# Optimization experiments

Hardware: AMD Instinct MI355X
Metric: run time of the kernel (lower is better)

Reference implementation:

```python
import jax, jax.numpy as jnp
import numpy as np

NUM_HEADS = 16
LN_EPS = 1e-05


def setup_inputs() -> dict:
    key = jax.random.key(0)
    ks = jax.random.split(key, 10)
    B, S, H = 2, 2048, 1024
    s = 1.0 / np.sqrt(H)
    return {
        "hidden_states": jax.random.normal(ks[0], (B, S, H), dtype=jnp.float32),
        "Wq": jax.random.normal(ks[1], (H, H), dtype=jnp.float32) * s,
        "bq": jax.random.normal(ks[2], (H,), dtype=jnp.float32) * 0.02,
        "Wk": jax.random.normal(ks[3], (H, H), dtype=jnp.float32) * s,
        "bk": jax.random.normal(ks[4], (H,), dtype=jnp.float32) * 0.02,
        "Wv": jax.random.normal(ks[5], (H, H), dtype=jnp.float32) * s,
        "bv": jax.random.normal(ks[6], (H,), dtype=jnp.float32) * 0.02,
        "Wd": jax.random.normal(ks[7], (H, H), dtype=jnp.float32) * s,
        "bd": jax.random.normal(ks[8], (H,), dtype=jnp.float32) * 0.02,
        "ln_gamma": jnp.ones((H,), dtype=jnp.float32),
        "ln_beta": jnp.zeros((H,), dtype=jnp.float32),
    }


def reference(hidden_states, Wq, bq, Wk, bk, Wv, bv, Wd, bd, ln_gamma, ln_beta):
    B, S, H = hidden_states.shape
    nh = NUM_HEADS
    hd = H // nh

    # QKV projections (torch Linear: x @ W.T + b), split heads -> [B, nh, S, hd]
    def proj(W, b):
        y = jnp.einsum('bsh,oh->bso', hidden_states, W) + b
        return y.reshape(B, S, nh, hd).transpose(0, 2, 1, 3)

    q = proj(Wq, bq)
    k = proj(Wk, bk)
    v = proj(Wv, bv)

    # scaled dot-product attention: [B, nh, S, S]
    scores = jnp.einsum('bhqd,bhkd->bhqk', q, k) / jnp.sqrt(jnp.float32(hd))
    probs = jax.nn.softmax(scores, axis=-1)
    ctx = jnp.einsum('bhqk,bhkd->bhqd', probs, v)  # [B, nh, S, hd]
    ctx = ctx.transpose(0, 2, 1, 3).reshape(B, S, H)

    # output dense + residual + LayerNorm
    attn_out = jnp.einsum('bsh,oh->bso', ctx, Wd) + bd
    x = attn_out + hidden_states
    mu = jnp.mean(x, axis=-1, keepdims=True)
    var = jnp.mean(jnp.square(x - mu), axis=-1, keepdims=True)
    return (x - mu) * jax.lax.rsqrt(var + LN_EPS) * ln_gamma + ln_beta
```

## Files before the change

kernel.cpp:

```cpp
#include <hip/hip_runtime.h>

constexpr int kH    = 1024;
constexpr int kSEQ  = 2048;
constexpr int kBATCH= 2;
constexpr int kNH   = 16;
constexpr int kHD   = 64;
constexpr int kM    = 4096;

typedef _Float16 h8  __attribute__((ext_vector_type(8)));
typedef _Float16 h4  __attribute__((ext_vector_type(4)));
typedef float   f32x4 __attribute__((ext_vector_type(4)));

static __device__ __forceinline__ f32x4 mfma16(h8 a, h8 b, f32x4 c) {
  return __builtin_amdgcn_mfma_f32_16x16x32_f16(a, b, c, 0, 0, 0);
}

static __device__ __forceinline__ void gll16(const _Float16* g, _Float16* l) {
  __builtin_amdgcn_global_load_lds(
      (const __attribute__((address_space(1))) void*)g,
      (__attribute__((address_space(3))) void*)l, 16, 0, 0);
}

#define QSCALE 0.18033688011112042f
#define C0INIT (-5.770780163555854f)

__global__ __launch_bounds__(256) void cvt_all(
    const float* __restrict__ X,  const float* __restrict__ Wq,
    const float* __restrict__ Wk, const float* __restrict__ Wv,
    const float* __restrict__ Wd,
    _Float16* __restrict__ Xh,  _Float16* __restrict__ Wqh,
    _Float16* __restrict__ Wkh, _Float16* __restrict__ Wvh,
    _Float16* __restrict__ Wdh)
{
  int i = blockIdx.x * 256 + threadIdx.x;
  const float* src; _Float16* dst; int off;
  if (i < (kM * kH) / 4) {
    src = X; dst = Xh; off = i;
  } else {
    int j = i - (kM * kH) / 4;
    int w = j >> 18;
    off = j & 262143;
    src = (w == 0) ? Wq : (w == 1) ? Wk : (w == 2) ? Wv : Wd;
    dst = (w == 0) ? Wqh : (w == 1) ? Wkh : (w == 2) ? Wvh : Wdh;
  }
  float4 v = reinterpret_cast<const float4*>(src)[off];
  h4 o;
  o[0] = (_Float16)v.x; o[1] = (_Float16)v.y;
  o[2] = (_Float16)v.z; o[3] = (_Float16)v.w;
  reinterpret_cast<h4*>(dst)[off] = o;
}

__global__ __launch_bounds__(256) void qkv_gemm(
    const _Float16* __restrict__ Xh,
    const _Float16* __restrict__ Wq, const _Float16* __restrict__ Wk,
    const _Float16* __restrict__ Wv,
    const float* __restrict__ bq, const float* __restrict__ bk,
    const float* __restrict__ bv,
    _Float16* __restrict__ Qo, _Float16* __restrict__ Ko, _Float16* __restrict__ Vo)
{
  const int proj = blockIdx.z;
  const _Float16* W   = (proj == 0) ? Wq : ((proj == 1) ? Wk : Wv);
  const float*    bias= (proj == 0) ? bq : ((proj == 1) ? bk : bv);
  _Float16*       Out = (proj == 0) ? Qo : ((proj == 1) ? Ko : Vo);

  const int m0 = blockIdx.y * 128, n0 = blockIdx.x * 128;
  __shared__ __align__(16) _Float16 As[128 * 32];
  __shared__ __align__(16) _Float16 Bs[128 * 32];

  const int tid  = threadIdx.x;
  const int wave = tid >> 6, lane = tid & 63, quad = lane >> 4, l16 = lane & 15;
  const int mw = (wave & 1) * 64, nw = (wave >> 1) * 64;

  f32x4 acc[4][4] = {};
  const int grow = wave * 32 + (lane >> 2);
  const int gcol = (lane & 3) * 8;
  const _Float16* Ag = Xh + (size_t)(m0 + grow) * kH + gcol;
  const _Float16* Bg = W  + (size_t)(n0 + grow) * kH + gcol;
  _Float16* AsW = As + wave * 1024;
  _Float16* BsW = Bs + wave * 1024;

  for (int k0 = 0; k0 < kH; k0 += 32) {
    gll16(Ag + k0,            AsW);
    gll16(Ag + 16 * kH + k0,  AsW + 512);
    gll16(Bg + k0,            BsW);
    gll16(Bg + 16 * kH + k0,  BsW + 512);
    __syncthreads();
    h8 af[4], bf[4];
    #pragma unroll
    for (int mi = 0; mi < 4; ++mi)
      af[mi] = *reinterpret_cast<const h8*>(&As[(mw + mi * 16 + l16) * 32 + quad * 8]);
    #pragma unroll
    for (int ni = 0; ni < 4; ++ni)
      bf[ni] = *reinterpret_cast<const h8*>(&Bs[(nw + ni * 16 + l16) * 32 + quad * 8]);
    #pragma unroll
    for (int mi = 0; mi < 4; ++mi)
      #pragma unroll
      for (int ni = 0; ni < 4; ++ni)
        acc[mi][ni] = mfma16(af[mi], bf[ni], acc[mi][ni]);
    __syncthreads();
  }

  #pragma unroll
  for (int mi = 0; mi < 4; ++mi)
  #pragma unroll
  for (int ni = 0; ni < 4; ++ni) {
    const int ng = n0 + nw + ni * 16 + l16;
    const float bv_ = bias[ng];
    const int hh = ng >> 6, dd = ng & 63;
    #pragma unroll
    for (int r = 0; r < 4; ++r) {
      const int mg = m0 + mw + mi * 16 + quad * 4 + r;
      float val = acc[mi][ni][r] + bv_;
      if (proj == 0) val *= QSCALE;
      const int bb = mg >> 11, srow = mg & 2047;
      Out[(((size_t)(bb * kNH + hh) * kSEQ) + srow) * kHD + dd] = (_Float16)val;
    }
  }
}

__global__ __launch_bounds__(256) void vtrans(const _Float16* __restrict__ V,
                                              _Float16* __restrict__ Vt)
{
  const int st = blockIdx.x;
  const int bh = blockIdx.y;
  __shared__ __align__(16) _Float16 Lt[64][72];
  const int t = threadIdx.x, r = t >> 2, c = (t & 3) * 16;
  const _Float16* src = V + (size_t)bh * kSEQ * kHD + (size_t)(st * 64 + r) * kHD + c;
  h8 p0 = *reinterpret_cast<const h8*>(src);
  h8 p1 = *reinterpret_cast<const h8*>(src + 8);
  #pragma unroll
  for (int e = 0; e < 8; ++e) Lt[c + e][r] = p0[e];
  #pragma unroll
  for (int e = 0; e < 8; ++e) Lt[c + 8 + e][r] = p1[e];
  __syncthreads();
  _Float16* dst = Vt + (size_t)bh * kHD * kSEQ + (size_t)r * kSEQ + st * 64 + c;
  *reinterpret_cast<h8*>(dst)     = *reinterpret_cast<const h8*>(&Lt[r][c]);
  *reinterpret_cast<h8*>(dst + 8) = *reinterpret_cast<const h8*>(&Lt[r][c + 8]);
}

__global__ __launch_bounds__(256, 2) void attn_kernel(
    const _Float16* __restrict__ Q, const _Float16* __restrict__ K,
    const _Float16* __restrict__ Vt, _Float16* __restrict__ Ctx)
{
  const int qt = blockIdx.x, bh = blockIdx.y;
  const int tid = threadIdx.x;
  const int wave = tid >> 6, lane = tid & 63, quad = lane >> 4, l16 = lane & 15;
  const int sw = l16 & 7;

  __shared__ __align__(16) _Float16 Kl[128 * 64];
  __shared__ __align__(16) _Float16 Vl[64 * 128];
  __shared__ __align__(16) _Float16 Pl[4 * 32 * 128];

  const _Float16* Qb = Q  + (size_t)bh * kSEQ * kHD;
  const _Float16* Kb = K  + (size_t)bh * kSEQ * kHD;
  const _Float16* Vb = Vt + (size_t)bh * kHD * kSEQ;

  const int qbase = qt * 128 + wave * 32;
  h8 qf[2][2];
  #pragma unroll
  for (int qh = 0; qh < 2; ++qh)
    #pragma unroll
    for (int dh = 0; dh < 2; ++dh)
      qf[qh][dh] = *reinterpret_cast<const h8*>(
          &Qb[(size_t)(qbase + qh * 16 + l16) * kHD + dh * 32 + quad * 8]);

  const int krow = wave * 32 + (lane >> 3);
  const int kcg  = (lane & 7) ^ ((lane >> 3) & 7);
  const _Float16* Kg0 = Kb + (size_t)krow * kHD + kcg * 8;
  _Float16* KlW = Kl + wave * 2048;
  const int vrow = wave * 16 + (lane >> 4);
  _Float16* VlW = Vl + wave * 2048;
  _Float16* PlW = Pl + wave * (32 * 128);

  float l_acc0 = 0.f, l_acc1 = 0.f;
  f32x4 o[2][4] = {};

  for (int kt = 0; kt < kSEQ / 128; ++kt) {
    __syncthreads();
    #pragma unroll
    for (int i = 0; i < 4; ++i)
      gll16(Kg0 + (size_t)kt * (128 * 64) + i * (8 * 64), KlW + i * 512);
    #pragma unroll
    for (int i = 0; i < 4; ++i) {
      const int d = vrow + i * 4;
      const int c = (lane & 15) ^ (d & 7);
      gll16(Vb + (size_t)d * kSEQ + kt * 128 + c * 8, VlW + i * 512);
    }
    __syncthreads();

    f32x4 s[8][2];
    #pragma unroll
    for (int nt = 0; nt < 8; ++nt) {
      const int keyl = nt * 16 + l16;
      h8 ka0 = *reinterpret_cast<const h8*>(&Kl[keyl * 64 + ((quad    ) ^ sw) * 8]);
      h8 ka1 = *reinterpret_cast<const h8*>(&Kl[keyl * 64 + ((quad + 4) ^ sw) * 8]);
      #pragma unroll
      for (int qh = 0; qh < 2; ++qh) {
        f32x4 a = {C0INIT, C0INIT, C0INIT, C0INIT};
        a = mfma16(ka0, qf[qh][0], a);
        a = mfma16(ka1, qf[qh][1], a);
        s[nt][qh] = a;
      }
    }
    #pragma unroll
    for (int nt = 0; nt < 8; ++nt)
      #pragma unroll
      for (int qh = 0; qh < 2; ++qh) {
        float e0 = exp2f(s[nt][qh][0]);
        float e1 = exp2f(s[nt][qh][1]);
        float e2 = exp2f(s[nt][qh][2]);
        float e3 = exp2f(s[nt][qh][3]);
        float t4 = (e0 + e1) + (e2 + e3);
        if (qh == 0) l_acc0 += t4; else l_acc1 += t4;
        h4 pp;
        pp[0] = (_Float16)e0; pp[1] = (_Float16)e1;
        pp[2] = (_Float16)e2; pp[3] = (_Float16)e3;
        const int c16 = (nt * 2 + (quad >> 1)) ^ sw;
        *reinterpret_cast<h4*>(
            &PlW[(qh * 16 + l16) * 128 + c16 * 8 + (quad & 1) * 4]) = pp;
      }
    #pragma unroll
    for (int kc = 0; kc < 4; ++kc) {
      const int cs = ((kc * 4 + quad) ^ sw) * 8;
      h8 pa0 = *reinterpret_cast<const h8*>(&PlW[l16 * 128 + cs]);
      h8 pa1 = *reinterpret_cast<const h8*>(&PlW[(16 + l16) * 128 + cs]);
      #pragma unroll
      for (int dt = 0; dt < 4; ++dt) {
        h8 vbf = *reinterpret_cast<const h8*>(&Vl[(dt * 16 + l16) * 128 + cs]);
        o[0][dt] = mfma16(pa0, vbf, o[0][dt]);
        o[1][dt] = mfma16(pa1, vbf, o[1][dt]);
      }
    }
  }

  float li[2] = {l_acc0, l_acc1};
  #pragma unroll
  for (int qh = 0; qh < 2; ++qh) {
    li[qh] += __shfl_xor(li[qh], 16);
    li[qh] += __shfl_xor(li[qh], 32);
    li[qh] = 1.f / li[qh];
  }
  const int b = bh >> 4, hh = bh & 15;
  #pragma unroll
  for (int qh = 0; qh < 2; ++qh)
    #pragma unroll
    for (int r = 0; r < 4; ++r) {
      const float linv = __shfl(li[qh], quad * 4 + r);
      const int srow = qbase + qh * 16 + quad * 4 + r;
      #pragma unroll
      for (int dt = 0; dt < 4; ++dt) {
        const int col = hh * kHD + dt * 16 + l16;
        Ctx[((size_t)(b * kSEQ + srow)) * kH + col] =
            (_Float16)(o[qh][dt][r] * linv);
      }
    }
}

__global__ __launch_bounds__(256) void dense_gemm(
    const _Float16* __restrict__ A, const _Float16* __restrict__ W,
    const float* __restrict__ bias, const float* __restrict__ resid,
    float* __restrict__ Out)
{
  const int m0 = blockIdx.y * 128, n0 = blockIdx.x * 128;
  __shared__ __align__(16) _Float16 As[128 * 32];
  __shared__ __align__(16) _Float16 Bs[128 * 32];
  const int tid  = threadIdx.x;
  const int wave = tid >> 6, lane = tid & 63, quad = lane >> 4, l16 = lane & 15;
  const int mw = (wave & 1) * 64, nw = (wave >> 1) * 64;
  f32x4 acc[4][4] = {};
  const int grow = wave * 32 + (lane >> 2);
  const int gcol = (lane & 3) * 8;
  const _Float16* Ag = A + (size_t)(m0 + grow) * kH + gcol;
  const _Float16* Bg = W + (size_t)(n0 + grow) * kH + gcol;
  _Float16* AsW = As + wave * 1024;
  _Float16* BsW = Bs + wave * 1024;

  for (int k0 = 0; k0 < kH; k0 += 32) {
    gll16(Ag + k0,           AsW);
    gll16(Ag + 16 * kH + k0, AsW + 512);
    gll16(Bg + k0,           BsW);
    gll16(Bg + 16 * kH + k0, BsW + 512);
    __syncthreads();
    h8 af[4], bf[4];
    #pragma unroll
    for (int mi = 0; mi < 4; ++mi)
      af[mi] = *reinterpret_cast<const h8*>(&As[(mw + mi * 16 + l16) * 32 + quad * 8]);
    #pragma unroll
    for (int ni = 0; ni < 4; ++ni)
      bf[ni] = *reinterpret_cast<const h8*>(&Bs[(nw + ni * 16 + l16) * 32 + quad * 8]);
    #pragma unroll
    for (int mi = 0; mi < 4; ++mi)
      #pragma unroll
      for (int ni = 0; ni < 4; ++ni)
        acc[mi][ni] = mfma16(af[mi], bf[ni], acc[mi][ni]);
    __syncthreads();
  }
  #pragma unroll
  for (int mi = 0; mi < 4; ++mi)
  #pragma unroll
  for (int ni = 0; ni < 4; ++ni) {
    const int ng = n0 + nw + ni * 16 + l16;
    const float bv_ = bias[ng];
    #pragma unroll
    for (int r = 0; r < 4; ++r) {
      const int mg = m0 + mw + mi * 16 + quad * 4 + r;
      Out[(size_t)mg * kH + ng] = acc[mi][ni][r] + bv_ + resid[(size_t)mg * kH + ng];
    }
  }
}

__global__ __launch_bounds__(256) void ln_kernel(const float* __restrict__ Tmp,
    const float* __restrict__ gamma, const float* __restrict__ beta,
    float* __restrict__ out)
{
  const int row = blockIdx.x;
  const float4 v = reinterpret_cast<const float4*>(Tmp + (size_t)row * kH)[threadIdx.x];
  float s  = v.x + v.y + v.z + v.w;
  float ss = v.x * v.x + v.y * v.y + v.z * v.z + v.w * v.w;
  #pragma unroll
  for (int off = 32; off > 0; off >>= 1) {
    s  += __shfl_down(s, off);
    ss += __shfl_down(ss, off);
  }
  __shared__ float red[8];
  const int wave = threadIdx.x >> 6, lane = threadIdx.x & 63;
  if (lane == 0) { red[wave] = s; red[4 + wave] = ss; }
  __syncthreads();
  s  = red[0] + red[1] + red[2] + red[3];
  ss = red[4] + red[5] + red[6] + red[7];
  const float mu   = s * (1.f / kH);
  const float var  = ss * (1.f / kH) - mu * mu;
  const float rstd = rsqrtf(var + 1e-5f);
  const float4 g  = reinterpret_cast<const float4*>(gamma)[threadIdx.x];
  const float4 bb = reinterpret_cast<const float4*>(beta)[threadIdx.x];
  float4 o;
  o.x = (v.x - mu) * rstd * g.x + bb.x;
  o.y = (v.y - mu) * rstd * g.y + bb.y;
  o.z = (v.z - mu) * rstd * g.z + bb.z;
  o.w = (v.w - mu) * rstd * g.w + bb.w;
  reinterpret_cast<float4*>(out + (size_t)row * kH)[threadIdx.x] = o;
}

extern "C" void kernel_launch(void* const* d_in, const int* in_sizes, int n_in,
                              void* d_out, int out_size, void* d_ws, size_t ws_size,
                              hipStream_t stream) {
  const float* hs    = (const float*)d_in[0];
  const float* Wq    = (const float*)d_in[1];
  const float* bq    = (const float*)d_in[2];
  const float* Wk    = (const float*)d_in[3];
  const float* bk    = (const float*)d_in[4];
  const float* Wv    = (const float*)d_in[5];
  const float* bv    = (const float*)d_in[6];
  const float* Wd    = (const float*)d_in[7];
  const float* bd    = (const float*)d_in[8];
  const float* gamma = (const float*)d_in[9];
  const float* beta  = (const float*)d_in[10];
  float* out = (float*)d_out;

  char* ws = (char*)d_ws;
  _Float16* Xh  = (_Float16*)(ws + 0);
  _Float16* Wqh = (_Float16*)(ws + 8388608);
  _Float16* Wkh = (_Float16*)(ws + 10485760);
  _Float16* Wvh = (_Float16*)(ws + 12582912);
  _Float16* Wdh = (_Float16*)(ws + 14680064);
  _Float16* Qh  = (_Float16*)(ws + 16777216);
  _Float16* Kh  = (_Float16*)(ws + 25165824);
  _Float16* Vh  = (_Float16*)(ws + 33554432);
  _Float16* Ch  = (_Float16*)(ws + 41943040);
  _Float16* Vtb = Xh;
  float*    Tmp = (float*)Qh;

  cvt_all<<<8192, 256, 0, stream>>>(hs, Wq, Wk, Wv, Wd, Xh, Wqh, Wkh, Wvh, Wdh);
  qkv_gemm<<<dim3(kH / 128, kM / 128, 3), 256, 0, stream>>>(
      Xh, Wqh, Wkh, Wvh, bq, bk, bv, Qh, Kh, Vh);
  vtrans<<<dim3(kSEQ / 64, kBATCH * kNH), 256, 0, stream>>>(Vh, Vtb);
  attn_kernel<<<dim3(kSEQ / 128, kBATCH * kNH), 256, 0, stream>>>(Qh, Kh, Vtb, Ch);
  dense_gemm<<<dim3(kH / 128, kM / 128), 256, 0, stream>>>(Ch, Wdh, bd, hs, Tmp);
  ln_kernel<<<kM, 256, 0, stream>>>(Tmp, gamma, beta, out);
}
```

Baseline: 237.4 us.

## Double-buffer LDS tiles in GEMMs and attention, shrink attention key tile

Both the QKV and dense GEMM kernels now double-buffer their A/B shared-memory tiles. The next k-slice is prefetched with global_load_lds right after a single barrier, replacing the previous load-sync-compute-sync loop. The attention kernel halves its key tile from 128 to 64, double-buffers the K and V tiles with the same prefetch pattern, and raises its occupancy hint from 2 to 3 blocks. The aim is to overlap global loads with MFMA work and cut barriers. In exchange the GEMMs use twice the LDS, the attention kernel runs twice as many loop iterations, and tighter launch bounds may pressure registers.

```diff
diff --git a/kernel.cpp b/kernel.cpp
--- a/kernel.cpp
+++ b/kernel.cpp
@@ -50,7 +50,7 @@
   reinterpret_cast<h4*>(dst)[off] = o;
 }
 
-__global__ __launch_bounds__(256) void qkv_gemm(
+__global__ __launch_bounds__(256, 2) void qkv_gemm(
     const _Float16* __restrict__ Xh,
     const _Float16* __restrict__ Wq, const _Float16* __restrict__ Wk,
     const _Float16* __restrict__ Wv,
@@ -64,8 +64,8 @@
   _Float16*       Out = (proj == 0) ? Qo : ((proj == 1) ? Ko : Vo);
 
   const int m0 = blockIdx.y * 128, n0 = blockIdx.x * 128;
-  __shared__ __align__(16) _Float16 As[128 * 32];
-  __shared__ __align__(16) _Float16 Bs[128 * 32];
+  __shared__ __align__(16) _Float16 As[2][128 * 32];
+  __shared__ __align__(16) _Float16 Bs[2][128 * 32];
 
   const int tid  = threadIdx.x;
   const int wave = tid >> 6, lane = tid & 63, quad = lane >> 4, l16 = lane & 15;
@@ -76,28 +76,36 @@
   const int gcol = (lane & 3) * 8;
   const _Float16* Ag = Xh + (size_t)(m0 + grow) * kH + gcol;
   const _Float16* Bg = W  + (size_t)(n0 + grow) * kH + gcol;
-  _Float16* AsW = As + wave * 1024;
-  _Float16* BsW = Bs + wave * 1024;
-
-  for (int k0 = 0; k0 < kH; k0 += 32) {
-    gll16(Ag + k0,            AsW);
-    gll16(Ag + 16 * kH + k0,  AsW + 512);
-    gll16(Bg + k0,            BsW);
-    gll16(Bg + 16 * kH + k0,  BsW + 512);
+
+  {
+    gll16(Ag,            &As[0][wave * 1024]);
+    gll16(Ag + 16 * kH,  &As[0][wave * 1024 + 512]);
+    gll16(Bg,            &Bs[0][wave * 1024]);
+    gll16(Bg + 16 * kH,  &Bs[0][wave * 1024 + 512]);
+  }
+
+  for (int k = 0; k < 32; ++k) {
+    const int cur = k & 1;
     __syncthreads();
+    if (k < 31) {
+      const int k0 = (k + 1) * 32, nb = cur ^ 1;
+      gll16(Ag + k0,           &As[nb][wave * 1024]);
+      gll16(Ag + 16 * kH + k0, &As[nb][wave * 1024 + 512]);
+      gll16(Bg + k0,           &Bs[nb][wave * 1024]);
+      gll16(Bg + 16 * kH + k0, &Bs[nb][wave * 1024 + 512]);
+    }
     h8 af[4], bf[4];
     #pragma unroll
     for (int mi = 0; mi < 4; ++mi)
-      af[mi] = *reinterpret_cast<const h8*>(&As[(mw + mi * 16 + l16) * 32 + quad * 8]);
+      af[mi] = *reinterpret_cast<const h8*>(&As[cur][(mw + mi * 16 + l16) * 32 + quad * 8]);
     #pragma unroll
     for (int ni = 0; ni < 4; ++ni)
-      bf[ni] = *reinterpret_cast<const h8*>(&Bs[(nw + ni * 16 + l16) * 32 + quad * 8]);
+      bf[ni] = *reinterpret_cast<const h8*>(&Bs[cur][(nw + ni * 16 + l16) * 32 + quad * 8]);
     #pragma unroll
     for (int mi = 0; mi < 4; ++mi)
       #pragma unroll
       for (int ni = 0; ni < 4; ++ni)
         acc[mi][ni] = mfma16(af[mi], bf[ni], acc[mi][ni]);
-    __syncthreads();
   }
 
   #pragma unroll
@@ -138,7 +146,7 @@
   *reinterpret_cast<h8*>(dst + 8) = *reinterpret_cast<const h8*>(&Lt[r][c + 8]);
 }
 
-__global__ __launch_bounds__(256, 2) void attn_kernel(
+__global__ __launch_bounds__(256, 3) void attn_kernel(
     const _Float16* __restrict__ Q, const _Float16* __restrict__ K,
     const _Float16* __restrict__ Vt, _Float16* __restrict__ Ctx)
 {
@@ -147,9 +155,9 @@
   const int wave = tid >> 6, lane = tid & 63, quad = lane >> 4, l16 = lane & 15;
   const int sw = l16 & 7;
 
-  __shared__ __align__(16) _Float16 Kl[128 * 64];
-  __shared__ __align__(16) _Float16 Vl[64 * 128];
-  __shared__ __align__(16) _Float16 Pl[4 * 32 * 128];
+  __shared__ __align__(16) _Float16 Kl[2][64 * 64];
+  __shared__ __align__(16) _Float16 Vl[2][64 * 64];
+  __shared__ __align__(16) _Float16 Pl[4][32 * 64];
 
   const _Float16* Qb = Q  + (size_t)bh * kSEQ * kHD;
   const _Float16* Kb = K  + (size_t)bh * kSEQ * kHD;
@@ -164,36 +172,43 @@
       qf[qh][dh] = *reinterpret_cast<const h8*>(
           &Qb[(size_t)(qbase + qh * 16 + l16) * kHD + dh * 32 + quad * 8]);
 
-  const int krow = wave * 32 + (lane >> 3);
-  const int kcg  = (lane & 7) ^ ((lane >> 3) & 7);
-  const _Float16* Kg0 = Kb + (size_t)krow * kHD + kcg * 8;
-  _Float16* KlW = Kl + wave * 2048;
-  const int vrow = wave * 16 + (lane >> 4);
-  _Float16* VlW = Vl + wave * 2048;
-  _Float16* PlW = Pl + wave * (32 * 128);
+  const int srow0  = lane >> 3;
+  const int schunk = (lane & 7) ^ srow0;
+  const int krow   = wave * 16 + srow0;
+  const _Float16* Kg = Kb + (size_t)krow * kHD + schunk * 8;
+  const _Float16* Vg = Vb + (size_t)krow * kSEQ + schunk * 8;
+  _Float16* PlW = Pl[wave];
 
   float l_acc0 = 0.f, l_acc1 = 0.f;
   f32x4 o[2][4] = {};
 
-  for (int kt = 0; kt < kSEQ / 128; ++kt) {
+  {
+    gll16(Kg,                 &Kl[0][(wave * 16) * 64]);
+    gll16(Kg + 8 * kHD,       &Kl[0][(wave * 16 + 8) * 64]);
+    gll16(Vg,                 &Vl[0][(wave * 16) * 64]);
+    gll16(Vg + 8 * kSEQ,      &Vl[0][(wave * 16 + 8) * 64]);
+  }
+
+  for (int kt = 0; kt < kSEQ / 64; ++kt) {
+    const int cur = kt & 1;
     __syncthreads();
-    #pragma unroll
-    for (int i = 0; i < 4; ++i)
-      gll16(Kg0 + (size_t)kt * (128 * 64) + i * (8 * 64), KlW + i * 512);
-    #pragma unroll
-    for (int i = 0; i < 4; ++i) {
-      const int d = vrow + i * 4;
-      const int c = (lane & 15) ^ (d & 7);
-      gll16(Vb + (size_t)d * kSEQ + kt * 128 + c * 8, VlW + i * 512);
-    }
-    __syncthreads();
-
-    f32x4 s[8][2];
-    #pragma unroll
-    for (int nt = 0; nt < 8; ++nt) {
+    if (kt + 1 < kSEQ / 64) {
+      const int nb = cur ^ 1;
+      const size_t ko = (size_t)(kt + 1) * 64;
+      gll16(Kg + ko * kHD,             &Kl[nb][(wave * 16) * 64]);
+      gll16(Kg + (ko + 8) * kHD,       &Kl[nb][(wave * 16 + 8) * 64]);
+      gll16(Vg + ko,                   &Vl[nb][(wave * 16) * 64]);
+      gll16(Vg + 8 * kSEQ + ko,        &Vl[nb][(wave * 16 + 8) * 64]);
+    }
+    const _Float16* Kc = Kl[cur];
+    const _Float16* Vc = Vl[cur];
+
+    f32x4 s[4][2];
+    #pragma unroll
+    for (int nt = 0; nt < 4; ++nt) {
       const int keyl = nt * 16 + l16;
-      h8 ka0 = *reinterpret_cast<const h8*>(&Kl[keyl * 64 + ((quad    ) ^ sw) * 8]);
-      h8 ka1 = *reinterpret_cast<const h8*>(&Kl[keyl * 64 + ((quad + 4) ^ sw) * 8]);
+      h8 ka0 = *reinterpret_cast<const h8*>(&Kc[keyl * 64 + ((quad     ) ^ sw) * 8]);
+      h8 ka1 = *reinterpret_cast<const h8*>(&Kc[keyl * 64 + ((quad ^ 4) ^ sw) * 8]);
       #pragma unroll
       for (int qh = 0; qh < 2; ++qh) {
         f32x4 a = {C0INIT, C0INIT, C0INIT, C0INIT};
@@ -203,7 +218,7 @@
       }
     }
     #pragma unroll
-    for (int nt = 0; nt < 8; ++nt)
+    for (int nt = 0; nt < 4; ++nt)
       #pragma unroll
       for (int qh = 0; qh < 2; ++qh) {
         float e0 = exp2f(s[nt][qh][0]);
@@ -215,18 +230,17 @@
         h4 pp;
         pp[0] = (_Float16)e0; pp[1] = (_Float16)e1;
         pp[2] = (_Float16)e2; pp[3] = (_Float16)e3;
-        const int c16 = (nt * 2 + (quad >> 1)) ^ sw;
-        *reinterpret_cast<h4*>(
-            &PlW[(qh * 16 + l16) * 128 + c16 * 8 + (quad & 1) * 4]) = pp;
+        const int c8 = (nt * 2 + (quad >> 1)) ^ sw;
+        *reinterpret_cast<h4*>(&PlW[(qh * 16 + l16) * 64 + c8 * 8 + (quad & 1) * 4]) = pp;
       }
     #pragma unroll
-    for (int kc = 0; kc < 4; ++kc) {
+    for (int kc = 0; kc < 2; ++kc) {
       const int cs = ((kc * 4 + quad) ^ sw) * 8;
-      h8 pa0 = *reinterpret_cast<const h8*>(&PlW[l16 * 128 + cs]);
-      h8 pa1 = *reinterpret_cast<const h8*>(&PlW[(16 + l16) * 128 + cs]);
+      h8 pa0 = *reinterpret_cast<const h8*>(&PlW[l16 * 64 + cs]);
+      h8 pa1 = *reinterpret_cast<const h8*>(&PlW[(16 + l16) * 64 + cs]);
       #pragma unroll
       for (int dt = 0; dt < 4; ++dt) {
-        h8 vbf = *reinterpret_cast<const h8*>(&Vl[(dt * 16 + l16) * 128 + cs]);
+        h8 vbf = *reinterpret_cast<const h8*>(&Vc[(dt * 16 + l16) * 64 + cs]);
         o[0][dt] = mfma16(pa0, vbf, o[0][dt]);
         o[1][dt] = mfma16(pa1, vbf, o[1][dt]);
       }
@@ -256,14 +270,14 @@
     }
 }
 
-__global__ __launch_bounds__(256) void dense_gemm(
+__global__ __launch_bounds__(256, 2) void dense_gemm(
     const _Float16* __restrict__ A, const _Float16* __restrict__ W,
     const float* __restrict__ bias, const float* __restrict__ resid,
     float* __restrict__ Out)
 {
   const int m0 = blockIdx.y * 128, n0 = blockIdx.x * 128;
-  __shared__ __align__(16) _Float16 As[128 * 32];
-  __shared__ __align__(16) _Float16 Bs[128 * 32];
+  __shared__ __align__(16) _Float16 As[2][128 * 32];
+  __shared__ __align__(16) _Float16 Bs[2][128 * 32];
   const int tid  = threadIdx.x;
   const int wave = tid >> 6, lane = tid & 63, quad = lane >> 4, l16 = lane & 15;
   const int mw = (wave & 1) * 64, nw = (wave >> 1) * 64;
@@ -272,28 +286,36 @@
   const int gcol = (lane & 3) * 8;
   const _Float16* Ag = A + (size_t)(m0 + grow) * kH + gcol;
   const _Float16* Bg = W + (size_t)(n0 + grow) * kH + gcol;
-  _Float16* AsW = As + wave * 1024;
-  _Float16* BsW = Bs + wave * 1024;
-
-  for (int k0 = 0; k0 < kH; k0 += 32) {
-    gll16(Ag + k0,           AsW);
-    gll16(Ag + 16 * kH + k0, AsW + 512);
-    gll16(Bg + k0,           BsW);
-    gll16(Bg + 16 * kH + k0, BsW + 512);
+
+  {
+    gll16(Ag,           &As[0][wave * 1024]);
+    gll16(Ag + 16 * kH, &As[0][wave * 1024 + 512]);
+    gll16(Bg,           &Bs[0][wave * 1024]);
+    gll16(Bg + 16 * kH, &Bs[0][wave * 1024 + 512]);
+  }
+
+  for (int k = 0; k < 32; ++k) {
+    const int cur = k & 1;
     __syncthreads();
+    if (k < 31) {
+      const int k0 = (k + 1) * 32, nb = cur ^ 1;
+      gll16(Ag + k0,           &As[nb][wave * 1024]);
+      gll16(Ag + 16 * kH + k0, &As[nb][wave * 1024 + 512]);
+      gll16(Bg + k0,           &Bs[nb][wave * 1024]);
+      gll16(Bg + 16 * kH + k0, &Bs[nb][wave * 1024 + 512]);
+    }
     h8 af[4], bf[4];
     #pragma unroll
     for (int mi = 0; mi < 4; ++mi)
-      af[mi] = *reinterpret_cast<const h8*>(&As[(mw + mi * 16 + l16) * 32 + quad * 8]);
+      af[mi] = *reinterpret_cast<const h8*>(&As[cur][(mw + mi * 16 + l16) * 32 + quad * 8]);
     #pragma unroll
     for (int ni = 0; ni < 4; ++ni)
-      bf[ni] = *reinterpret_cast<const h8*>(&Bs[(nw + ni * 16 + l16) * 32 + quad * 8]);
+      bf[ni] = *reinterpret_cast<const h8*>(&Bs[cur][(nw + ni * 16 + l16) * 32 + quad * 8]);
     #pragma unroll
     for (int mi = 0; mi < 4; ++mi)
       #pragma unroll
       for (int ni = 0; ni < 4; ++ni)
         acc[mi][ni] = mfma16(af[mi], bf[ni], acc[mi][ni]);
-    __syncthreads();
   }
   #pragma unroll
   for (int mi = 0; mi < 4; ++mi)
```

After: 231.3 us. 2.6% less time.
